# Performance work log

Measured on AMD Instinct MI355X. Metric: run time of the kernel, lower is better.

## Reference

```python
import jax, jax.numpy as jnp
import numpy as np
from jax import lax

DN = ('NCDHW', 'OIDHW', 'NCDHW')

def conv3d(x, w, b=None):
    y = lax.conv_general_dilated(x, w, window_strides=(1, 1, 1), padding='SAME', dimension_numbers=DN)
    if b is not None:
        y = y + b[None, :, None, None, None]
    return y

def adaptive_conv(x, w):
    # x: [B,C,D,H,W]; w: [B,27,D,H,W] per-voxel 3x3x3 kernel weights
    B, C, D, H, W = x.shape
    xp = jnp.pad(x, ((0, 0), (0, 0), (1, 1), (1, 1), (1, 1)))
    out = jnp.zeros_like(x)
    idx = 0
    for i in range(3):
        for j in range(3):
            for k in range(3):
                out = out + xp[:, :, i:i + D, j:j + H, k:k + W] * w[:, idx][:, None]
                idx += 1
    return out

def setup_inputs() -> dict:
    key = jax.random.key(0)
    k1, k2, k3 = jax.random.split(key, 3)
    B, C, D, H, W = 1, 8, 128, 128, 128
    x = jax.random.normal(k1, (B, C, D, H, W), dtype=jnp.float32)
    w1 = jax.random.normal(k2, (8, 8, 3, 3, 3), dtype=jnp.float32) * 0.1
    b1 = jnp.zeros((8,), dtype=jnp.float32)
    w2 = jax.random.normal(k3, (27, 8, 3, 3, 3), dtype=jnp.float32) * 0.1
    return {"x": x, "w1": w1, "b1": b1, "w2": w2}

def reference(x, w1, b1, w2):
    # adaptive_block: per-voxel 27-tap weights from a small conv stack
    h = jax.nn.relu(conv3d(x, w1, b1))
    w = conv3d(h, w2)  # [B,27,D,H,W]
    # F.normalize(w, dim=1, p=1)
    n = jnp.sum(jnp.abs(w), axis=1, keepdims=True)
    w = w / jnp.maximum(n, 1e-12)
    out = x
    for _ in range(3):
        out = adaptive_conv(out, w)
    return out
```

## Files before the change

### kernel.cpp

```cpp
#include <hip/hip_runtime.h>
#include <hip/hip_bf16.h>

constexpr int HW2 = 16384;
constexpr int DHW = 2097152;

constexpr int PKG = 13;
constexpr int XT  = 130;

typedef short bf16x8 __attribute__((ext_vector_type(8)));
typedef float f32x4  __attribute__((ext_vector_type(4)));

__device__ inline unsigned short f2b(float f) {
  __hip_bfloat16 h = __float2bfloat16(f);
  return *(unsigned short*)&h;
}
__device__ inline float b2f(unsigned short u) {
  __hip_bfloat16 h = *(__hip_bfloat16*)&u;
  return __bfloat162float(h);
}

__global__ __launch_bounds__(256) void k_prep(
    const float* __restrict__ w1, const float* __restrict__ w2,
    unsigned short* __restrict__ Wpack2, unsigned short* __restrict__ Wpack1,
    float* __restrict__ g_ti, float* __restrict__ g_xi) {
  int i = blockIdx.x * 256 + threadIdx.x;
  if (i < 9216) {
    int j = i & 7;
    int lane = (i >> 3) & 63;
    int Mt = (i >> 9) & 1;
    int g2 = i >> 10;
    int s = g2 % 3, dx = g2 / 3;
    int oc = Mt * 16 + (lane & 15);
    int kr = s * 32 + (lane >> 4) * 8 + j;
    int ci = kr & 7, g = kr >> 3;
    float w = 0.f;
    if (oc < 27 && (g & 3) < 3) {
      int dzr = g >> 2, dyr = g & 3;
      w = w2[(oc * 8 + ci) * 27 + dzr * 9 + dyr * 3 + dx];
    }
    Wpack2[i] = f2b(w);
  }
  int jj = i - 9216;
  if (jj >= 0 && jj < 4608) {
    int j = jj & 7;
    int lane = (jj >> 3) & 63;
    int g2 = jj >> 9;
    int s = g2 % 3, dx = g2 / 3;
    int oc = lane & 15;
    int kr = s * 32 + (lane >> 4) * 8 + j;
    int ci = kr & 7, g = kr >> 3;
    float w = 0.f;
    if (oc < 8 && (g & 3) < 3) {
      int dzr = g >> 2, dyr = g & 3;
      w = w1[(oc * 8 + ci) * 27 + dzr * 9 + dyr * 3 + dx];
    }
    Wpack1[jj] = f2b(w);
  }
  int gg = i - 13824;
  if (gg >= 0 && gg < 32) {
    float* p = (gg < 8)  ? (g_ti - 8 + gg)
             : (gg < 16) ? (g_ti + (size_t)8 * DHW + (gg - 8))
             : (gg < 24) ? (g_xi - 8 + (gg - 16))
                         : (g_xi + (size_t)8 * DHW + (gg - 24));
    *p = 0.f;
  }
}

__global__ __launch_bounds__(256) void k_xpose(
    const float* __restrict__ x, unsigned short* __restrict__ xb,
    float* __restrict__ xi) {
  int idx = blockIdx.x * 256 + threadIdx.x;
  float f[8];
  unsigned v[4];
#pragma unroll
  for (int p = 0; p < 4; ++p) {
    f[2 * p]     = x[(size_t)(2 * p) * DHW + idx];
    f[2 * p + 1] = x[(size_t)(2 * p + 1) * DHW + idx];
    unsigned lo = f2b(f[2 * p]);
    unsigned hi = f2b(f[2 * p + 1]);
    v[p] = lo | (hi << 16);
  }
  ((uint4*)xb)[idx] = make_uint4(v[0], v[1], v[2], v[3]);
  float4* xo = (float4*)(xi + (size_t)idx * 8);
  xo[0] = make_float4(f[0], f[1], f[2], f[3]);
  xo[1] = make_float4(f[4], f[5], f[6], f[7]);
}

#define STAGE_ROWS2(srcp)                                                  \
  {                                                                        \
    if (tid < 154) {                                                       \
      if (tid < 130) {                                                     \
        dst[tid * PKG + 12] = make_uint4(0u, 0u, 0u, 0u);                  \
      } else {                                                             \
        int k = tid - 130;                                                 \
        int sl = k >> 1, xih = (k & 1) ? 129 : 0;                          \
        dst[xih * PKG + sl] = make_uint4(0u, 0u, 0u, 0u);                  \
      }                                                                    \
    }                                                                      \
    const int gg = tid >> 7;                                               \
    const int xi_ = (tid & 127) + 1;                                       \
    const int xg_ = xi_ - 1;                                               \
    uint4 sv[6];                                                           \
    bool vld[6];                                                           \
    _Pragma("unroll")                                                      \
    for (int it = 0; it < 6; ++it) {                                       \
      const int g = gg + it * 2;                                           \
      const int dz = g >> 2, ry = g & 3;                                   \
      const int z = z0 + dz - 1, y = y0 + ry - 1;                          \
      vld[it] = ((unsigned)z < 128u) & ((unsigned)y < 128u);               \
      const int zz = vld[it] ? z : z0, yy = vld[it] ? y : y0;              \
      sv[it] = (srcp)[(zz * 128 + yy) * 128 + xg_];                        \
    }                                                                      \
    _Pragma("unroll")                                                      \
    for (int it = 0; it < 6; ++it) {                                       \
      const int g = gg + it * 2;                                           \
      uint4 v = vld[it] ? sv[it] : make_uint4(0u, 0u, 0u, 0u);             \
      dst[xi_ * PKG + g] = v;                                              \
    }                                                                      \
  }

__global__ __launch_bounds__(256, 3) void k_conv1m(
    const unsigned short* __restrict__ xb,
    const unsigned short* __restrict__ Wpack1,
    const float* __restrict__ b1, unsigned short* __restrict__ hb) {
  __shared__ __align__(16) unsigned short T[XT * PKG * 8];
  const int tid  = threadIdx.x;
  const int lane = tid & 63;
  const int wv   = tid >> 6;
  const int logical = (blockIdx.x & 7) * 1024 + (blockIdx.x >> 3);
  const int z0 = logical >> 6;
  const int y0 = (logical & 63) * 2;

  bf16x8 wf[3][3];
  {
    const bf16x8* wp = (const bf16x8*)Wpack1;
#pragma unroll
    for (int dx = 0; dx < 3; ++dx)
#pragma unroll
      for (int s = 0; s < 3; ++s)
        wf[dx][s] = wp[(dx * 3 + s) * 64 + lane];
  }

  const uint4* src = (const uint4*)xb;
  uint4* dst = (uint4*)T;
  STAGE_ROWS2(src);
  __syncthreads();

  f32x4 acc[2][2];
#pragma unroll
  for (int r = 0; r < 2; ++r)
#pragma unroll
    for (int nt = 0; nt < 2; ++nt) acc[r][nt] = (f32x4){0.f, 0.f, 0.f, 0.f};

  const int n = lane & 15;
  const int q = lane >> 4;
  const int xbase = wv * 32 + n;

#pragma unroll
  for (int dx = 0; dx < 3; ++dx) {
#pragma unroll
    for (int s = 0; s < 3; ++s) {
      bf16x8 bfr[2][2];
#pragma unroll
      for (int r = 0; r < 2; ++r)
#pragma unroll
        for (int nt = 0; nt < 2; ++nt) {
          int off = ((xbase + nt * 16 + dx) * PKG + (s * 4 + q + r)) * 8;
          bfr[r][nt] = *(const bf16x8*)&T[off];
        }
#pragma unroll
      for (int r = 0; r < 2; ++r)
#pragma unroll
        for (int nt = 0; nt < 2; ++nt)
          acc[r][nt] = __builtin_amdgcn_mfma_f32_16x16x32_bf16(
              wf[dx][s], bfr[r][nt], acc[r][nt], 0, 0, 0);
    }
  }

  if (q < 2) {
#pragma unroll
    for (int r = 0; r < 2; ++r) {
      const int voxrow = (z0 * 128 + y0 + r) * 128;
#pragma unroll
      for (int nt = 0; nt < 2; ++nt) {
        const int vox = voxrow + wv * 32 + nt * 16 + n;
        ushort4 o;
        o.x = f2b(fmaxf(acc[r][nt][0] + b1[q * 4 + 0], 0.f));
        o.y = f2b(fmaxf(acc[r][nt][1] + b1[q * 4 + 1], 0.f));
        o.z = f2b(fmaxf(acc[r][nt][2] + b1[q * 4 + 2], 0.f));
        o.w = f2b(fmaxf(acc[r][nt][3] + b1[q * 4 + 3], 0.f));
        *(ushort4*)(hb + (size_t)vox * 8 + q * 4) = o;
      }
    }
  }
}

__global__ __launch_bounds__(256, 2) void k_conv2(
    const unsigned short* __restrict__ hb,
    const unsigned short* __restrict__ Wpack2,
    unsigned short* __restrict__ wn) {
  __shared__ __align__(16) unsigned short T[XT * PKG * 8];
  const int tid  = threadIdx.x;
  const int lane = tid & 63;
  const int wv   = tid >> 6;
  const int logical = (blockIdx.x & 7) * 1024 + (blockIdx.x >> 3);
  const int z0 = logical >> 6;
  const int y0 = (logical & 63) * 2;

  bf16x8 wf[3][3][2];
  {
    const bf16x8* wp = (const bf16x8*)Wpack2;
#pragma unroll
    for (int dx = 0; dx < 3; ++dx)
#pragma unroll
      for (int s = 0; s < 3; ++s)
#pragma unroll
        for (int mt = 0; mt < 2; ++mt)
          wf[dx][s][mt] = wp[((dx * 3 + s) * 2 + mt) * 64 + lane];
  }

  const uint4* src = (const uint4*)hb;
  uint4* dst = (uint4*)T;
  STAGE_ROWS2(src);
  __syncthreads();

  f32x4 acc[2][2][2];
#pragma unroll
  for (int r = 0; r < 2; ++r)
#pragma unroll
    for (int nt = 0; nt < 2; ++nt)
#pragma unroll
      for (int mt = 0; mt < 2; ++mt)
        acc[r][nt][mt] = (f32x4){0.f, 0.f, 0.f, 0.f};

  const int n = lane & 15;
  const int q = lane >> 4;
  const int xbase = wv * 32 + n;

#pragma unroll
  for (int dx = 0; dx < 3; ++dx) {
#pragma unroll
    for (int s = 0; s < 3; ++s) {
      bf16x8 bfr[2][2];
#pragma unroll
      for (int r = 0; r < 2; ++r)
#pragma unroll
        for (int nt = 0; nt < 2; ++nt) {
          int off = ((xbase + nt * 16 + dx) * PKG + (s * 4 + q + r)) * 8;
          bfr[r][nt] = *(const bf16x8*)&T[off];
        }
#pragma unroll
      for (int r = 0; r < 2; ++r)
#pragma unroll
        for (int mt = 0; mt < 2; ++mt)
#pragma unroll
          for (int nt = 0; nt < 2; ++nt)
            acc[r][nt][mt] = __builtin_amdgcn_mfma_f32_16x16x32_bf16(
                wf[dx][s][mt], bfr[r][nt], acc[r][nt][mt], 0, 0, 0);
    }
  }

#pragma unroll
  for (int r = 0; r < 2; ++r) {
    const int voxrow = (z0 * 128 + y0 + r) * 128;
#pragma unroll
    for (int nt = 0; nt < 2; ++nt) {
      float ns = 0.f;
#pragma unroll
      for (int rr = 0; rr < 4; ++rr) ns += fabsf(acc[r][nt][0][rr]);
#pragma unroll
      for (int rr = 0; rr < 4; ++rr) {
        int oc = 16 + q * 4 + rr;
        ns += (oc < 27) ? fabsf(acc[r][nt][1][rr]) : 0.f;
      }
      ns += __shfl_xor(ns, 16);
      ns += __shfl_xor(ns, 32);
      float sc = 1.f / fmaxf(ns, 1e-12f);
      const int vox = voxrow + wv * 32 + nt * 16 + n;
#pragma unroll
      for (int rr = 0; rr < 4; ++rr) {
        int oc = q * 4 + rr;
        wn[(size_t)oc * DHW + vox] = f2b(acc[r][nt][0][rr] * sc);
      }
#pragma unroll
      for (int rr = 0; rr < 4; ++rr) {
        int oc = 16 + q * 4 + rr;
        if (oc < 27)
          wn[(size_t)oc * DHW + vox] = f2b(acc[r][nt][1][rr] * sc);
      }
    }
  }
}

constexpr int APITCH = 2112;
__device__ inline int swz7(int off) { return off ^ (((off >> 7) & 7) << 4); }

template <int FINAL>
__global__ __launch_bounds__(256, 1) void k_adapt8(
    const float* __restrict__ in, const unsigned short* __restrict__ wn,
    float* __restrict__ out) {
  __shared__ __align__(16) char S[36 * APITCH];
  const int tid = threadIdx.x;
  const int logical = (blockIdx.x & 7) * 256 + (blockIdx.x >> 3);
  const int xh  = logical & 1;
  const int typ = (logical >> 1) & 31;
  const int tzp = logical >> 6;
  const int x0 = xh * 64, y0 = typ * 4, z0 = tzp * 4;

  const int th = tid >> 7;
  const int kcol = tid & 127;
  const int wbyte = swz7(32 + kcol * 16);
#pragma unroll 1
  for (int ib = 0; ib < 2; ++ib) {
    uint4 stg[9];
#pragma unroll
    for (int i = 0; i < 9; ++i) {
      const int r = 2 * (ib * 9 + i) + th;
      const int r6 = r / 6;
      const int zs = min(max(z0 - 1 + r6, 0), 127);
      const int ys = min(max(y0 - 1 + (r - r6 * 6), 0), 127);
      stg[i] = *(const uint4*)(in + (size_t)(zs * 128 + ys) * 1024 +
                               x0 * 8 + kcol * 4);
    }
#pragma unroll
    for (int i = 0; i < 9; ++i) {
      const int r = 2 * (ib * 9 + i) + th;
      *(uint4*)(S + r * APITCH + wbyte) = stg[i];
    }
  }
  if (tid < 144) {
    const int hr = tid >> 2;
    const int hp = tid & 3;
    const int r6 = hr / 6;
    const int zs = min(max(z0 - 1 + r6, 0), 127);
    const int ys = min(max(y0 - 1 + (hr - r6 * 6), 0), 127);
    const int fo = (hp < 2) ? ((x0 - 1) * 8 + hp * 4)
                            : ((x0 + 64) * 8 + (hp - 2) * 4);
    uint4 v = *(const uint4*)(in + (size_t)(zs * 128 + ys) * 1024 + fo);
    const bool zero = xh ? (hp >= 2) : (hp < 2);
    if (zero) v = make_uint4(0u, 0u, 0u, 0u);
    const int sb = (hp < 2) ? (hp * 16) : (65 * 32 + (hp - 2) * 16);
    *(uint4*)(S + hr * APITCH + swz7(sb)) = v;
  }
  __syncthreads();

  const int xp = tid & 31;
  const int yp = (tid >> 5) & 1;
  const int zo = tid >> 6;
  const int Y = y0 + 2 * yp;
  const int Z = z0 + zo;

  unsigned zokm = 0;
#pragma unroll
  for (int d = 0; d < 3; ++d)
    zokm |= ((unsigned)(Z + d - 1) < 128u) ? (1u << d) : 0u;
  bool yok[2][3];
#pragma unroll
  for (int oy = 0; oy < 2; ++oy)
#pragma unroll
    for (int d = 0; d < 3; ++d)
      yok[oy][d] = (unsigned)(Y + oy + d - 1) < 128u;

  int soff[4][2];
#pragma unroll
  for (int j = 0; j < 4; ++j)
#pragma unroll
    for (int h = 0; h < 2; ++h)
      soff[j][h] = swz7((2 * xp + j) * 32 + h * 16);

  const size_t voxp0 = (size_t)(Z * 128 + Y) * 128 + x0 + 2 * xp;

  f32x4 acc[2][2][2];
#pragma unroll
  for (int oy = 0; oy < 2; ++oy)
#pragma unroll
    for (int ox = 0; ox < 2; ++ox)
#pragma unroll
      for (int h = 0; h < 2; ++h)
        acc[oy][ox][h] = (f32x4){0.f, 0.f, 0.f, 0.f};

#pragma unroll 1
  for (int dz = 0; dz < 3; ++dz) {
    const char* Rz = S + ((zo + dz) * 6 + 2 * yp) * APITCH;
    const unsigned short* wz = wn + (size_t)dz * 9 * DHW;
    const bool zv = (zokm >> dz) & 1u;
#pragma unroll
    for (int yr = 0; yr < 4; ++yr) {
      const char* R = Rz + yr * APITCH;
      f32x4 W[4][2];
#pragma unroll
      for (int j = 0; j < 4; ++j)
#pragma unroll
        for (int h = 0; h < 2; ++h)
          W[j][h] = *(const f32x4*)(R + soff[j][h]);
#pragma unroll
      for (int oy = 0; oy < 2; ++oy) {
        const int dy = yr - oy;
        if (dy >= 0 && dy < 3) {
          const bool val = zv && yok[oy][dy];
          const size_t voxp = voxp0 + (size_t)oy * 128;
#pragma unroll
          for (int dxi = 0; dxi < 3; ++dxi) {
            const unsigned u = *(const unsigned*)(
                wz + (size_t)(dy * 3 + dxi) * DHW + voxp);
            const float w0 = val ? b2f((unsigned short)(u & 0xffffu)) : 0.f;
            const float w1 = val ? b2f((unsigned short)(u >> 16)) : 0.f;
#pragma unroll
            for (int h = 0; h < 2; ++h)
#pragma unroll
              for (int c = 0; c < 4; ++c) {
                acc[oy][0][h][c] = fmaf(W[dxi][h][c], w0, acc[oy][0][h][c]);
                acc[oy][1][h][c] =
                    fmaf(W[dxi + 1][h][c], w1, acc[oy][1][h][c]);
              }
          }
        }
      }
    }
  }

  if (FINAL) {
#pragma unroll
    for (int oy = 0; oy < 2; ++oy) {
      const size_t voxp = voxp0 + (size_t)oy * 128;
#pragma unroll
      for (int h = 0; h < 2; ++h)
#pragma unroll
        for (int c = 0; c < 4; ++c) {
          float2 o = make_float2(acc[oy][0][h][c], acc[oy][1][h][c]);
          *(float2*)(out + (size_t)(h * 4 + c) * DHW + voxp) = o;
        }
    }
  } else {
#pragma unroll
    for (int oy = 0; oy < 2; ++oy) {
      const size_t voxp = voxp0 + (size_t)oy * 128;
      f32x4* op = (f32x4*)(out + voxp * 8);
      op[0] = acc[oy][0][0];
      op[1] = acc[oy][0][1];
      op[2] = acc[oy][1][0];
      op[3] = acc[oy][1][1];
    }
  }
}

extern "C" void kernel_launch(void* const* d_in, const int* in_sizes, int n_in,
                              void* d_out, int out_size, void* d_ws, size_t ws_size,
                              hipStream_t stream) {
  const float* x  = (const float*)d_in[0];
  const float* w1 = (const float*)d_in[1];
  const float* b1 = (const float*)d_in[2];
  const float* w2 = (const float*)d_in[3];
  float* out = (float*)d_out;

  char* ws = (char*)d_ws;
  unsigned short* xb = (unsigned short*)ws;
  unsigned short* hb = (unsigned short*)(ws + (size_t)8 * DHW * 2);
  float* ti = (float*)(ws + 256);
  unsigned short* wn = (unsigned short*)(ws + (size_t)16 * DHW * 2 + 4096);
  float* xi = (float*)(ws + (size_t)16 * DHW * 2 + 4096 +
                       (size_t)27 * DHW * 2 + 8192);
  unsigned short* Wpack2 =
      (unsigned short*)((char*)xi + (size_t)8 * DHW * 4 + 16384);
  unsigned short* Wpack1 = Wpack2 + 9216;

  dim3 blk(256);
  k_prep<<<55, blk, 0, stream>>>(w1, w2, Wpack2, Wpack1, ti, xi);
  k_xpose<<<DHW / 256, blk, 0, stream>>>(x, xb, xi);
  k_conv1m<<<128 * 64, blk, 0, stream>>>(xb, Wpack1, b1, hb);
  k_conv2<<<128 * 64, blk, 0, stream>>>(hb, Wpack2, wn);
  k_adapt8<0><<<2048, blk, 0, stream>>>(xi, wn, ti);
  k_adapt8<0><<<2048, blk, 0, stream>>>(ti, wn, xi);
  k_adapt8<1><<<2048, blk, 0, stream>>>(xi, wn, out);
}
```

Measured before the change: 358.1 us.

## Tile conv1/conv2 over four y-rows per block to cut halo restaging

Each conv block now computes four y-rows instead of two. It stages a 3x6 row halo in LDS with a new packing stride of 25, which lowers the halo overhead per output row from 3x to 1.5x in global loads and LDS fills. The grid is halved to match. In conv2 the weight fragments are now loaded per dx inside the loop instead of all up front, and the occupancy hint is raised to 3 to offset the larger accumulator array. The cost is more accumulator registers and LDS per block.

```diff
diff --git a/kernel.cpp b/kernel.cpp
--- a/kernel.cpp
+++ b/kernel.cpp
@@ -4,7 +4,7 @@
 constexpr int HW2 = 16384;
 constexpr int DHW = 2097152;
 
-constexpr int PKG = 13;
+constexpr int PKQ = 25;
 constexpr int XT  = 130;
 
 typedef short bf16x8 __attribute__((ext_vector_type(8)));
@@ -86,36 +86,43 @@
   xo[1] = make_float4(f[4], f[5], f[6], f[7]);
 }
 
-#define STAGE_ROWS2(srcp)                                                  \
+#define STAGE_QUAD(srcp)                                                   \
   {                                                                        \
-    if (tid < 154) {                                                       \
-      if (tid < 130) {                                                     \
-        dst[tid * PKG + 12] = make_uint4(0u, 0u, 0u, 0u);                  \
-      } else {                                                             \
-        int k = tid - 130;                                                 \
-        int sl = k >> 1, xih = (k & 1) ? 129 : 0;                          \
-        dst[xih * PKG + sl] = make_uint4(0u, 0u, 0u, 0u);                  \
+    if (tid < 195) {                                                       \
+      _Pragma("unroll")                                                    \
+      for (int k = 0; k < 2; ++k) {                                        \
+        const int c = tid * 2 + k;                              \
+        const int dzz = c / 130;                                           \
+        const int xih = c - 130 * dzz;                                     \
+        dst[xih * PKQ + dzz * 8 + 6] = make_uint4(0u, 0u, 0u, 0u);         \
       }                                                                    \
     }                                                                      \
-    const int gg = tid >> 7;                                               \
-    const int xi_ = (tid & 127) + 1;                                       \
-    const int xg_ = xi_ - 1;                                               \
-    uint4 sv[6];                                                           \
-    bool vld[6];                                                           \
+    if (tid < 36) {                                                        \
+      const int sl = tid >> 1;                                  \
+      const int dzz = sl / 6, ryy = sl - 6 * dzz;                          \
+      const int xih = (tid & 1) ? 129 : 0;                                 \
+      dst[xih * PKQ + dzz * 8 + ryy] = make_uint4(0u, 0u, 0u, 0u);         \
+    }                                                                      \
+    const int th_ = tid >> 7;                                              \
+    const int col_ = tid & 127;                                            \
+    const int xi_ = col_ + 1;                                              \
+    uint4 sv[9];                                                           \
+    bool vld[9];                                                           \
     _Pragma("unroll")                                                      \
-    for (int it = 0; it < 6; ++it) {                                       \
-      const int g = gg + it * 2;                                           \
-      const int dz = g >> 2, ry = g & 3;                                   \
-      const int z = z0 + dz - 1, y = y0 + ry - 1;                          \
+    for (int it = 0; it < 9; ++it) {                                       \
+      const int row = 2 * it + th_;                             \
+      const int dzz = row / 6, ryy = row - 6 * dzz;                        \
+      const int z = z0 + dzz - 1, y = y0 + ryy - 1;                        \
       vld[it] = ((unsigned)z < 128u) & ((unsigned)y < 128u);               \
       const int zz = vld[it] ? z : z0, yy = vld[it] ? y : y0;              \
-      sv[it] = (srcp)[(zz * 128 + yy) * 128 + xg_];                        \
+      sv[it] = (srcp)[(zz * 128 + yy) * 128 + col_];                       \
     }                                                                      \
     _Pragma("unroll")                                                      \
-    for (int it = 0; it < 6; ++it) {                                       \
-      const int g = gg + it * 2;                                           \
+    for (int it = 0; it < 9; ++it) {                                       \
+      const int row = 2 * it + th_;                                        \
+      const int dzz = row / 6, ryy = row - 6 * dzz;                        \
       uint4 v = vld[it] ? sv[it] : make_uint4(0u, 0u, 0u, 0u);             \
-      dst[xi_ * PKG + g] = v;                                              \
+      dst[xi_ * PKQ + dzz * 8 + ryy] = v;                                  \
     }                                                                      \
   }
 
@@ -123,13 +130,13 @@
     const unsigned short* __restrict__ xb,
     const unsigned short* __restrict__ Wpack1,
     const float* __restrict__ b1, unsigned short* __restrict__ hb) {
-  __shared__ __align__(16) unsigned short T[XT * PKG * 8];
+  __shared__ __align__(16) unsigned short T[XT * PKQ * 8];
   const int tid  = threadIdx.x;
   const int lane = tid & 63;
   const int wv   = tid >> 6;
-  const int logical = (blockIdx.x & 7) * 1024 + (blockIdx.x >> 3);
-  const int z0 = logical >> 6;
-  const int y0 = (logical & 63) * 2;
+  const int logical = (blockIdx.x & 7) * 512 + (blockIdx.x >> 3);
+  const int z0 = logical >> 5;
+  const int y0 = (logical & 31) * 4;
 
   bf16x8 wf[3][3];
   {
@@ -143,12 +150,12 @@
 
   const uint4* src = (const uint4*)xb;
   uint4* dst = (uint4*)T;
-  STAGE_ROWS2(src);
+  STAGE_QUAD(src);
   __syncthreads();
 
-  f32x4 acc[2][2];
-#pragma unroll
-  for (int r = 0; r < 2; ++r)
+  f32x4 acc[4][2];
+#pragma unroll
+  for (int r = 0; r < 4; ++r)
 #pragma unroll
     for (int nt = 0; nt < 2; ++nt) acc[r][nt] = (f32x4){0.f, 0.f, 0.f, 0.f};
 
@@ -160,16 +167,16 @@
   for (int dx = 0; dx < 3; ++dx) {
 #pragma unroll
     for (int s = 0; s < 3; ++s) {
-      bf16x8 bfr[2][2];
-#pragma unroll
-      for (int r = 0; r < 2; ++r)
+      bf16x8 bfr[4][2];
+#pragma unroll
+      for (int r = 0; r < 4; ++r)
 #pragma unroll
         for (int nt = 0; nt < 2; ++nt) {
-          int off = ((xbase + nt * 16 + dx) * PKG + (s * 4 + q + r)) * 8;
+          int off = ((xbase + nt * 16 + dx) * PKQ + (s * 8 + q + r)) * 8;
           bfr[r][nt] = *(const bf16x8*)&T[off];
         }
 #pragma unroll
-      for (int r = 0; r < 2; ++r)
+      for (int r = 0; r < 4; ++r)
 #pragma unroll
         for (int nt = 0; nt < 2; ++nt)
           acc[r][nt] = __builtin_amdgcn_mfma_f32_16x16x32_bf16(
@@ -179,7 +186,7 @@
 
   if (q < 2) {
 #pragma unroll
-    for (int r = 0; r < 2; ++r) {
+    for (int r = 0; r < 4; ++r) {
       const int voxrow = (z0 * 128 + y0 + r) * 128;
 #pragma unroll
       for (int nt = 0; nt < 2; ++nt) {
@@ -195,38 +202,26 @@
   }
 }
 
-__global__ __launch_bounds__(256, 2) void k_conv2(
+__global__ __launch_bounds__(256, 3) void k_conv2(
     const unsigned short* __restrict__ hb,
     const unsigned short* __restrict__ Wpack2,
     unsigned short* __restrict__ wn) {
-  __shared__ __align__(16) unsigned short T[XT * PKG * 8];
+  __shared__ __align__(16) unsigned short T[XT * PKQ * 8];
   const int tid  = threadIdx.x;
   const int lane = tid & 63;
   const int wv   = tid >> 6;
-  const int logical = (blockIdx.x & 7) * 1024 + (blockIdx.x >> 3);
-  const int z0 = logical >> 6;
-  const int y0 = (logical & 63) * 2;
-
-  bf16x8 wf[3][3][2];
-  {
-    const bf16x8* wp = (const bf16x8*)Wpack2;
-#pragma unroll
-    for (int dx = 0; dx < 3; ++dx)
-#pragma unroll
-      for (int s = 0; s < 3; ++s)
-#pragma unroll
-        for (int mt = 0; mt < 2; ++mt)
-          wf[dx][s][mt] = wp[((dx * 3 + s) * 2 + mt) * 64 + lane];
-  }
+  const int logical = (blockIdx.x & 7) * 512 + (blockIdx.x >> 3);
+  const int z0 = logical >> 5;
+  const int y0 = (logical & 31) * 4;
 
   const uint4* src = (const uint4*)hb;
   uint4* dst = (uint4*)T;
-  STAGE_ROWS2(src);
+  STAGE_QUAD(src);
   __syncthreads();
 
-  f32x4 acc[2][2][2];
-#pragma unroll
-  for (int r = 0; r < 2; ++r)
+  f32x4 acc[4][2][2];
+#pragma unroll
+  for (int r = 0; r < 4; ++r)
 #pragma unroll
     for (int nt = 0; nt < 2; ++nt)
 #pragma unroll
@@ -236,32 +231,39 @@
   const int n = lane & 15;
   const int q = lane >> 4;
   const int xbase = wv * 32 + n;
+  const bf16x8* wp = (const bf16x8*)Wpack2;
 
 #pragma unroll
   for (int dx = 0; dx < 3; ++dx) {
+    bf16x8 wf[3][2];
+#pragma unroll
+    for (int s = 0; s < 3; ++s)
+#pragma unroll
+      for (int mt = 0; mt < 2; ++mt)
+        wf[s][mt] = wp[((dx * 3 + s) * 2 + mt) * 64 + lane];
 #pragma unroll
     for (int s = 0; s < 3; ++s) {
-      bf16x8 bfr[2][2];
-#pragma unroll
-      for (int r = 0; r < 2; ++r)
+      bf16x8 bfr[4][2];
+#pragma unroll
+      for (int r = 0; r < 4; ++r)
 #pragma unroll
         for (int nt = 0; nt < 2; ++nt) {
-          int off = ((xbase + nt * 16 + dx) * PKG + (s * 4 + q + r)) * 8;
+          int off = ((xbase + nt * 16 + dx) * PKQ + (s * 8 + q + r)) * 8;
           bfr[r][nt] = *(const bf16x8*)&T[off];
         }
 #pragma unroll
-      for (int r = 0; r < 2; ++r)
+      for (int r = 0; r < 4; ++r)
 #pragma unroll
         for (int mt = 0; mt < 2; ++mt)
 #pragma unroll
           for (int nt = 0; nt < 2; ++nt)
             acc[r][nt][mt] = __builtin_amdgcn_mfma_f32_16x16x32_bf16(
-                wf[dx][s][mt], bfr[r][nt], acc[r][nt][mt], 0, 0, 0);
-    }
-  }
-
-#pragma unroll
-  for (int r = 0; r < 2; ++r) {
+                wf[s][mt], bfr[r][nt], acc[r][nt][mt], 0, 0, 0);
+    }
+  }
+
+#pragma unroll
+  for (int r = 0; r < 4; ++r) {
     const int voxrow = (z0 * 128 + y0 + r) * 128;
 #pragma unroll
     for (int nt = 0; nt < 2; ++nt) {
@@ -467,8 +469,8 @@
   dim3 blk(256);
   k_prep<<<55, blk, 0, stream>>>(w1, w2, Wpack2, Wpack1, ti, xi);
   k_xpose<<<DHW / 256, blk, 0, stream>>>(x, xb, xi);
-  k_conv1m<<<128 * 64, blk, 0, stream>>>(xb, Wpack1, b1, hb);
-  k_conv2<<<128 * 64, blk, 0, stream>>>(hb, Wpack2, wn);
+  k_conv1m<<<128 * 32, blk, 0, stream>>>(xb, Wpack1, b1, hb);
+  k_conv2<<<128 * 32, blk, 0, stream>>>(hb, Wpack2, wn);
   k_adapt8<0><<<2048, blk, 0, stream>>>(xi, wn, ti);
   k_adapt8<0><<<2048, blk, 0, stream>>>(ti, wn, xi);
   k_adapt8<1><<<2048, blk, 0, stream>>>(xi, wn, out);
```

Measured after the change: 363.1 us. No clear change (+1.4%).

## Stage conv and adaptive tiles via direct global-to-LDS loads

Applied to the files above, without the earlier changes.

Replaces register-staged global loads followed by LDS stores with the global_load_lds builtin, which writes 16-byte chunks straight into shared memory, in the two conv kernels and in the adaptive kernel. The conv LDS tile is transposed from x-major (pitch 13) to row-major (pitch 130) so each wavefront writes one contiguous run. In the adaptive kernel the swizzle is applied on the global-address side instead of the LDS side. The aim is to save VGPRs and instructions during staging, at the cost of relying on a correct swizzle inversion and on waitcnt handling before the barrier, and possibly changing LDS bank-conflict patterns on MFMA operand reads.

```diff
diff --git a/kernel.cpp b/kernel.cpp
--- a/kernel.cpp
+++ b/kernel.cpp
@@ -4,8 +4,7 @@
 constexpr int HW2 = 16384;
 constexpr int DHW = 2097152;
 
-constexpr int PKG = 13;
-constexpr int XT  = 130;
+constexpr int CPITCH = 130;
 
 typedef short bf16x8 __attribute__((ext_vector_type(8)));
 typedef float f32x4  __attribute__((ext_vector_type(4)));
@@ -17,6 +16,12 @@
 __device__ inline float b2f(unsigned short u) {
   __hip_bfloat16 h = *(__hip_bfloat16*)&u;
   return __bfloat162float(h);
+}
+
+__device__ inline void gld16(const void* g, void* l) {
+  __builtin_amdgcn_global_load_lds(
+      (const __attribute__((address_space(1))) unsigned int*)g,
+      (__attribute__((address_space(3))) unsigned int*)l, 16, 0, 0);
 }
 
 __global__ __launch_bounds__(256) void k_prep(
@@ -86,36 +91,30 @@
   xo[1] = make_float4(f[4], f[5], f[6], f[7]);
 }
 
-#define STAGE_ROWS2(srcp)                                                  \
+#define STAGE_G(srcp)                                                      \
   {                                                                        \
-    if (tid < 154) {                                                       \
-      if (tid < 130) {                                                     \
-        dst[tid * PKG + 12] = make_uint4(0u, 0u, 0u, 0u);                  \
+    uint4* dstc = (uint4*)T;                                               \
+    if (tid < 130) dstc[12 * CPITCH + tid] = make_uint4(0u, 0u, 0u, 0u);   \
+    if (tid < 24) {                                                        \
+      const int row = tid >> 1, xih = (tid & 1) ? 129 : 0;                 \
+      dstc[row * CPITCH + xih] = make_uint4(0u, 0u, 0u, 0u);               \
+    }                                                                      \
+    const int wv_ = tid >> 6;                                              \
+    const int l_  = tid & 63;                                              \
+    _Pragma("unroll")                                                      \
+    for (int i = 0; i < 6; ++i) {                                          \
+      const int t = wv_ + 4 * i;                                           \
+      const int row = t >> 1, hf = t & 1;                                  \
+      const int dz = row >> 2, ry = row & 3;                               \
+      const int z = z0 + dz - 1, y = y0 + ry - 1;                          \
+      char* lb = (char*)T + (size_t)(row * CPITCH + 1 + hf * 64) * 16;     \
+      if (((unsigned)z < 128u) & ((unsigned)y < 128u)) {                   \
+        const uint4* g = (srcp) + (size_t)(z * 128 + y) * 128 +            \
+                         hf * 64 + l_;                                     \
+        gld16((const void*)g, (void*)lb);                                  \
       } else {                                                             \
-        int k = tid - 130;                                                 \
-        int sl = k >> 1, xih = (k & 1) ? 129 : 0;                          \
-        dst[xih * PKG + sl] = make_uint4(0u, 0u, 0u, 0u);                  \
+        *(uint4*)(lb + l_ * 16) = make_uint4(0u, 0u, 0u, 0u);              \
       }                                                                    \
-    }                                                                      \
-    const int gg = tid >> 7;                                               \
-    const int xi_ = (tid & 127) + 1;                                       \
-    const int xg_ = xi_ - 1;                                               \
-    uint4 sv[6];                                                           \
-    bool vld[6];                                                           \
-    _Pragma("unroll")                                                      \
-    for (int it = 0; it < 6; ++it) {                                       \
-      const int g = gg + it * 2;                                           \
-      const int dz = g >> 2, ry = g & 3;                                   \
-      const int z = z0 + dz - 1, y = y0 + ry - 1;                          \
-      vld[it] = ((unsigned)z < 128u) & ((unsigned)y < 128u);               \
-      const int zz = vld[it] ? z : z0, yy = vld[it] ? y : y0;              \
-      sv[it] = (srcp)[(zz * 128 + yy) * 128 + xg_];                        \
-    }                                                                      \
-    _Pragma("unroll")                                                      \
-    for (int it = 0; it < 6; ++it) {                                       \
-      const int g = gg + it * 2;                                           \
-      uint4 v = vld[it] ? sv[it] : make_uint4(0u, 0u, 0u, 0u);             \
-      dst[xi_ * PKG + g] = v;                                              \
     }                                                                      \
   }
 
@@ -123,7 +122,7 @@
     const unsigned short* __restrict__ xb,
     const unsigned short* __restrict__ Wpack1,
     const float* __restrict__ b1, unsigned short* __restrict__ hb) {
-  __shared__ __align__(16) unsigned short T[XT * PKG * 8];
+  __shared__ __align__(16) unsigned short T[13 * CPITCH * 8];
   const int tid  = threadIdx.x;
   const int lane = tid & 63;
   const int wv   = tid >> 6;
@@ -142,8 +141,7 @@
   }
 
   const uint4* src = (const uint4*)xb;
-  uint4* dst = (uint4*)T;
-  STAGE_ROWS2(src);
+  STAGE_G(src);
   __syncthreads();
 
   f32x4 acc[2][2];
@@ -165,7 +163,7 @@
       for (int r = 0; r < 2; ++r)
 #pragma unroll
         for (int nt = 0; nt < 2; ++nt) {
-          int off = ((xbase + nt * 16 + dx) * PKG + (s * 4 + q + r)) * 8;
+          int off = ((s * 4 + q + r) * CPITCH + xbase + nt * 16 + dx) * 8;
           bfr[r][nt] = *(const bf16x8*)&T[off];
         }
 #pragma unroll
@@ -199,7 +197,7 @@
     const unsigned short* __restrict__ hb,
     const unsigned short* __restrict__ Wpack2,
     unsigned short* __restrict__ wn) {
-  __shared__ __align__(16) unsigned short T[XT * PKG * 8];
+  __shared__ __align__(16) unsigned short T[13 * CPITCH * 8];
   const int tid  = threadIdx.x;
   const int lane = tid & 63;
   const int wv   = tid >> 6;
@@ -220,8 +218,7 @@
   }
 
   const uint4* src = (const uint4*)hb;
-  uint4* dst = (uint4*)T;
-  STAGE_ROWS2(src);
+  STAGE_G(src);
   __syncthreads();
 
   f32x4 acc[2][2][2];
@@ -246,7 +243,7 @@
       for (int r = 0; r < 2; ++r)
 #pragma unroll
         for (int nt = 0; nt < 2; ++nt) {
-          int off = ((xbase + nt * 16 + dx) * PKG + (s * 4 + q + r)) * 8;
+          int off = ((s * 4 + q + r) * CPITCH + xbase + nt * 16 + dx) * 8;
           bfr[r][nt] = *(const bf16x8*)&T[off];
         }
 #pragma unroll
@@ -296,7 +293,7 @@
 __device__ inline int swz7(int off) { return off ^ (((off >> 7) & 7) << 4); }
 
 template <int FINAL>
-__global__ __launch_bounds__(256, 1) void k_adapt8(
+__global__ __launch_bounds__(256, 1) void k_adapt10(
     const float* __restrict__ in, const unsigned short* __restrict__ wn,
     float* __restrict__ out) {
   __shared__ __align__(16) char S[36 * APITCH];
@@ -307,25 +304,22 @@
   const int tzp = logical >> 6;
   const int x0 = xh * 64, y0 = typ * 4, z0 = tzp * 4;
 
-  const int th = tid >> 7;
-  const int kcol = tid & 127;
-  const int wbyte = swz7(32 + kcol * 16);
-#pragma unroll 1
-  for (int ib = 0; ib < 2; ++ib) {
-    uint4 stg[9];
-#pragma unroll
-    for (int i = 0; i < 9; ++i) {
-      const int r = 2 * (ib * 9 + i) + th;
+  {
+    const int wv_ = tid >> 6;
+    const int l_  = tid & 63;
+#pragma unroll
+    for (int i = 0; i < 18; ++i) {
+      const int t = wv_ + 4 * i;
+      const int r = t >> 1, hf = t & 1;
       const int r6 = r / 6;
       const int zs = min(max(z0 - 1 + r6, 0), 127);
       const int ys = min(max(y0 - 1 + (r - r6 * 6), 0), 127);
-      stg[i] = *(const uint4*)(in + (size_t)(zs * 128 + ys) * 1024 +
-                               x0 * 8 + kcol * 4);
-    }
-#pragma unroll
-    for (int i = 0; i < 9; ++i) {
-      const int r = 2 * (ib * 9 + i) + th;
-      *(uint4*)(S + r * APITCH + wbyte) = stg[i];
+      const int q = 32 + hf * 1024 + l_ * 16;
+      const int p = swz7(q);
+      const char* g = (const char*)in + (size_t)(zs * 128 + ys) * 4096 +
+                      (size_t)x0 * 32 + (p - 32);
+      char* lb = S + r * APITCH + 32 + hf * 1024;
+      gld16((const void*)g, (void*)lb);
     }
   }
   if (tid < 144) {
@@ -469,7 +463,7 @@
   k_xpose<<<DHW / 256, blk, 0, stream>>>(x, xb, xi);
   k_conv1m<<<128 * 64, blk, 0, stream>>>(xb, Wpack1, b1, hb);
   k_conv2<<<128 * 64, blk, 0, stream>>>(hb, Wpack2, wn);
-  k_adapt8<0><<<2048, blk, 0, stream>>>(xi, wn, ti);
-  k_adapt8<0><<<2048, blk, 0, stream>>>(ti, wn, xi);
-  k_adapt8<1><<<2048, blk, 0, stream>>>(xi, wn, out);
-}
+  k_adapt10<0><<<2048, blk, 0, stream>>>(xi, wn, ti);
+  k_adapt10<0><<<2048, blk, 0, stream>>>(ti, wn, xi);
+  k_adapt10<1><<<2048, blk, 0, stream>>>(xi, wn, out);
+}
```

Result: no change. 351.6 us (-1.8%).
